# Optimization experiments

Hardware: AMD Instinct MI355X
Metric: run time of the kernel (lower is better)

Reference implementation:

```python
import jax, jax.numpy as jnp
import numpy as np

EPS = 1e-5

def gcn_conv(x, src, dst, W, b, N):
    # PyG GCNConv with self-loops already appended to (src, dst):
    # out = D^{-1/2} (A+I) D^{-1/2} (x @ W) + b
    h = x @ W  # [N, F_out]
    deg = jax.ops.segment_sum(jnp.ones(dst.shape[0], h.dtype), dst, num_segments=N)
    dinv = jnp.where(deg > 0, jax.lax.rsqrt(deg), 0.0)
    norm = dinv[src] * dinv[dst]  # [E']
    msg = h[src] * norm[:, None]  # gather + scale
    out = jax.ops.segment_sum(msg, dst, num_segments=N)  # scatter-add
    return out + b

def layer_norm(x, gamma, beta):
    mu = jnp.mean(x, axis=-1, keepdims=True)
    var = jnp.mean((x - mu) ** 2, axis=-1, keepdims=True)
    return (x - mu) * jax.lax.rsqrt(var + EPS) * gamma + beta

def setup_inputs() -> dict:
    key = jax.random.key(0)
    ks = jax.random.split(key, 12)
    N, E, STEPS = 200000, 12800000, 4
    node = jax.random.normal(ks[0], (N, 3), dtype=jnp.float32)
    edges = jax.random.randint(ks[1], (2, E), 0, N, dtype=jnp.int64)
    W1 = jax.random.normal(ks[2], (3, 6), dtype=jnp.float32) * 0.5
    b1 = jnp.zeros((6,), jnp.float32)
    Wl = jax.random.normal(ks[3], (STEPS, 6, 6), dtype=jnp.float32) * 0.4
    bl = jnp.zeros((STEPS, 6), jnp.float32)
    gamma = jnp.ones((STEPS, 6), jnp.float32)
    beta = jnp.zeros((STEPS, 6), jnp.float32)
    Wfc = jax.random.normal(ks[4], (6, 3), dtype=jnp.float32) * 0.4
    bfc = jnp.zeros((3,), jnp.float32)
    return {"node": node, "edges": edges, "W1": W1, "b1": b1, "Wl": Wl,
            "bl": bl, "gamma": gamma, "beta": beta, "Wfc": Wfc, "bfc": bfc}

def reference(node, edges, W1, b1, Wl, bl, gamma, beta, Wfc, bfc):
    N = node.shape[0]
    loops = jnp.arange(N, dtype=edges.dtype)
    src = jnp.concatenate([edges[0], loops])  # add self-loops once
    dst = jnp.concatenate([edges[1], loops])
    x = gcn_conv(node, src, dst, W1, b1, N)
    steps = Wl.shape[0]
    for i in range(steps):
        x_res = x
        x = gcn_conv(x, src, dst, Wl[i], bl[i], N)
        x = layer_norm(x, gamma[i], beta[i])
        x = x + x_res
        x = jax.nn.relu(x)
    return x @ Wfc + bfc
```

## Files before the change

### kernel.cpp

```cpp
#include <hip/hip_runtime.h>
#include <hip/hip_fp16.h>
#include <cstdint>

#define EPSLN 1e-5f
#define NPB 256
#define NPB_SHIFT 8
#define MAXB 1024
#define TILE 16384
#define SRC_BITS 18
#define SRC_MASK 0x3FFFF
#define FCAP 17664
#define FK 35

__global__ __launch_bounds__(512) void k_init(int* __restrict__ bcur, int B, int cap) {
    int b = blockIdx.x * 512 + threadIdx.x;
    if (b < B) bcur[b] = b * cap;
}

__global__ __launch_bounds__(512) void k_scatter(const int* __restrict__ src,
                                                 const int* __restrict__ dst,
                                                 int* __restrict__ bcur,
                                                 unsigned* __restrict__ packed,
                                                 int E, int B) {
    __shared__ unsigned stg[TILE];
    __shared__ int hist[MAXB];
    __shared__ int lbase[MAXB + 1];
    __shared__ int sm[MAXB];
    int tid = threadIdx.x;
    int i0 = tid, i1 = tid + 512;
    hist[i0] = 0; hist[i1] = 0;
    __syncthreads();

    int beg = blockIdx.x * TILE;
    int end = min(beg + TILE, E);
    int cnt = end - beg;

    unsigned w[32];
    unsigned m[32];

    if (cnt == TILE && ((E & 3) == 0)) {
        const int4* d4 = (const int4*)(dst + beg);
        const int4* s4 = (const int4*)(src + beg);
#pragma unroll
        for (int k = 0; k < 8; ++k) {
            int4 d = d4[tid + k * 512];
            int4 s = s4[tid + k * 512];
            int b0 = d.x >> NPB_SHIFT, b1 = d.y >> NPB_SHIFT;
            int b2 = d.z >> NPB_SHIFT, b3 = d.w >> NPB_SHIFT;
            int r0 = atomicAdd(&hist[b0], 1);
            int r1 = atomicAdd(&hist[b1], 1);
            int r2 = atomicAdd(&hist[b2], 1);
            int r3 = atomicAdd(&hist[b3], 1);
            w[4 * k + 0] = ((unsigned)(d.x & (NPB - 1)) << SRC_BITS) | (unsigned)s.x;
            w[4 * k + 1] = ((unsigned)(d.y & (NPB - 1)) << SRC_BITS) | (unsigned)s.y;
            w[4 * k + 2] = ((unsigned)(d.z & (NPB - 1)) << SRC_BITS) | (unsigned)s.z;
            w[4 * k + 3] = ((unsigned)(d.w & (NPB - 1)) << SRC_BITS) | (unsigned)s.w;
            m[4 * k + 0] = ((unsigned)b0 << 14) | (unsigned)r0;
            m[4 * k + 1] = ((unsigned)b1 << 14) | (unsigned)r1;
            m[4 * k + 2] = ((unsigned)b2 << 14) | (unsigned)r2;
            m[4 * k + 3] = ((unsigned)b3 << 14) | (unsigned)r3;
        }
    } else {
#pragma unroll
        for (int k = 0; k < 32; ++k) {
            int i = beg + tid + k * 512;
            if (i < end) {
                int d = dst[i];
                int s = src[i];
                int bkt = d >> NPB_SHIFT;
                int r = atomicAdd(&hist[bkt], 1);
                w[k] = ((unsigned)(d & (NPB - 1)) << SRC_BITS) | (unsigned)s;
                m[k] = ((unsigned)bkt << 14) | (unsigned)r;
            } else {
                m[k] = 0xFFFFFFFFu;
            }
        }
    }
    __syncthreads();

    int v0 = hist[i0], v1 = hist[i1];
    sm[i0] = v0; sm[i1] = v1;
    __syncthreads();
    for (int off = 1; off < MAXB; off <<= 1) {
        int t0 = (i0 >= off) ? sm[i0 - off] : 0;
        int t1 = (i1 >= off) ? sm[i1 - off] : 0;
        __syncthreads();
        sm[i0] += t0; sm[i1] += t1;
        __syncthreads();
    }
    lbase[i0] = sm[i0] - v0;
    lbase[i1] = sm[i1] - v1;
    if (i0 < B) hist[i0] = v0 ? atomicAdd(&bcur[i0], v0) : 0;
    if (i1 < B) hist[i1] = v1 ? atomicAdd(&bcur[i1], v1) : 0;
    if (tid == 0) lbase[B] = cnt;
    __syncthreads();

#pragma unroll
    for (int k = 0; k < 32; ++k) {
        if (m[k] != 0xFFFFFFFFu) {
            int bkt = (int)(m[k] >> 14);
            int r   = (int)(m[k] & 16383u);
            stg[lbase[bkt] + r] = w[k];
        }
    }
    __syncthreads();

    int grp = tid >> 4;
    int gl  = tid & 15;
    for (int b = grp; b < B; b += 32) {
        int lb = lbase[b];
        int le = lbase[b + 1];
        int gb = hist[b];
        for (int j = lb + gl; j < le; j += 16)
            packed[gb + (j - lb)] = stg[j];
    }
}

__global__ __launch_bounds__(512) void k_fine(const int* __restrict__ bcur,
                                              const unsigned* __restrict__ packed,
                                              int* __restrict__ csr,
                                              int2* __restrict__ ptr2,
                                              float* __restrict__ dinv,
                                              float* __restrict__ sqd,
                                              const float* __restrict__ node,
                                              float* __restrict__ xs3,
                                              int N, int cap) {
    __shared__ unsigned stg[FCAP];
    __shared__ int hist[NPB];
    __shared__ int exs[NPB];
    int b = blockIdx.x;
    int tid = threadIdx.x;
    int beg = b * cap;
    int cnt = min(bcur[b] - beg, FCAP);
    if (tid < NPB) hist[tid] = 0;
    __syncthreads();

    unsigned w[FK];
    int r[FK];
#pragma unroll
    for (int k = 0; k < FK; ++k) {
        int i = tid + k * 512;
        if (i < cnt) {
            w[k] = packed[beg + i];
            r[k] = atomicAdd(&hist[w[k] >> SRC_BITS], 1);
        }
    }
    __syncthreads();

    int hv = 0;
    if (tid < NPB) { hv = hist[tid]; exs[tid] = hv; }
    __syncthreads();
    for (int off = 1; off < NPB; off <<= 1) {
        int t = 0;
        if (tid < NPB && tid >= off) t = exs[tid - off];
        __syncthreads();
        if (tid < NPB) exs[tid] += t;
        __syncthreads();
    }
    if (tid < NPB) {
        int ex = exs[tid] - hv;
        int v = b * NPB + tid;
        if (v < N) {
            ptr2[v] = make_int2(beg + ex, beg + ex + hv);
            float c = (float)(hv + 1);
            float di = rsqrtf(c);
            dinv[v] = di;
            sqd[v] = sqrtf(c);
            xs3[(size_t)v * 4 + 0] = di * node[(size_t)v * 3 + 0];
            xs3[(size_t)v * 4 + 1] = di * node[(size_t)v * 3 + 1];
            xs3[(size_t)v * 4 + 2] = di * node[(size_t)v * 3 + 2];
            xs3[(size_t)v * 4 + 3] = 0.f;
        }
        exs[tid] = ex;
    }
    __syncthreads();

#pragma unroll
    for (int k = 0; k < FK; ++k) {
        int i = tid + k * 512;
        if (i < cnt) {
            int dl = (int)(w[k] >> SRC_BITS);
            stg[exs[dl] + r[k]] = w[k] & SRC_MASK;
        }
    }
    __syncthreads();

    for (int j = tid; j < cnt; j += 512)
        csr[beg + j] = (int)stg[j];
}

template <int MODE>
__global__ __launch_bounds__(512) void k_conv(const int2* __restrict__ ptr2,
                                              const int* __restrict__ csr,
                                              const float* __restrict__ dinv,
                                              const float* __restrict__ sqd,
                                              const float* __restrict__ xs,
                                              const __half* __restrict__ xsh,
                                              const float* __restrict__ W,
                                              const float* __restrict__ b,
                                              const float* __restrict__ gamma,
                                              const float* __restrict__ beta,
                                              const float* __restrict__ Wfc,
                                              const float* __restrict__ bfc,
                                              float* __restrict__ xsout,
                                              __half* __restrict__ xhout,
                                              float* __restrict__ outfc,
                                              int N) {
    constexpr int F = (MODE == 0) ? 3 : 6;
    int wave = threadIdx.x >> 6;
    int lane = threadIdx.x & 63;
    int sub  = lane >> 4;
    int li   = lane & 15;
    int v = (blockIdx.x * 8 + wave) * 4 + sub;
    bool valid = v < N;
    int beg = 0, end = 0;
    if (valid) { int2 p = ptr2[v]; beg = p.x; end = p.y; }

    float a0 = 0.f, a1 = 0.f, a2 = 0.f, a3 = 0.f, a4 = 0.f, a5 = 0.f;
    float xr0 = 0.f, xr1 = 0.f, xr2 = 0.f, xr3 = 0.f, xr4 = 0.f, xr5 = 0.f;
    if constexpr (F == 3) {
        const float4* x4 = (const float4*)xs;
        if (valid && li == 0) { float4 p = x4[v]; a0 += p.x; a1 += p.y; a2 += p.z; }
        int i = beg + li;
        int last = end - 1;
        while (i < end) {
            int i1 = i + 16, i2 = i + 32, i3 = i + 48;
            int j0 = csr[i];
            int j1 = csr[min(i1, last)];
            int j2 = csr[min(i2, last)];
            int j3 = csr[min(i3, last)];
            float4 p0 = x4[j0];
            float4 p1 = x4[j1];
            float4 p2 = x4[j2];
            float4 p3 = x4[j3];
            a0 += p0.x; a1 += p0.y; a2 += p0.z;
            if (i1 < end) { a0 += p1.x; a1 += p1.y; a2 += p1.z; }
            if (i2 < end) { a0 += p2.x; a1 += p2.y; a2 += p2.z; }
            if (i3 < end) { a0 += p3.x; a1 += p3.y; a2 += p3.z; }
            i += 64;
        }
    } else {
        const float4* xh4 = (const float4*)xsh;
        if (valid && li == 0) {
            const float* rp = xs + (size_t)v * 8;
            float4 p = *(const float4*)rp;
            float2 q = *(const float2*)(rp + 4);
            xr0 = p.x; xr1 = p.y; xr2 = p.z; xr3 = p.w; xr4 = q.x; xr5 = q.y;
            a0 += xr0; a1 += xr1; a2 += xr2; a3 += xr3; a4 += xr4; a5 += xr5;
        }
        int i = beg + li;
        int last = end - 1;
        while (i < end) {
            int i1 = i + 16, i2 = i + 32, i3 = i + 48;
            int j0 = csr[i];
            int j1 = csr[min(i1, last)];
            int j2 = csr[min(i2, last)];
            int j3 = csr[min(i3, last)];
            float4 r0 = xh4[j0];
            float4 r1 = xh4[j1];
            float4 r2 = xh4[j2];
            float4 r3 = xh4[j3];
            {
                const __half2* h2 = (const __half2*)&r0;
                float2 p0 = __half22float2(h2[0]);
                float2 p1 = __half22float2(h2[1]);
                float2 p2 = __half22float2(h2[2]);
                a0 += p0.x; a1 += p0.y; a2 += p1.x; a3 += p1.y; a4 += p2.x; a5 += p2.y;
            }
            if (i1 < end) {
                const __half2* h2 = (const __half2*)&r1;
                float2 p0 = __half22float2(h2[0]);
                float2 p1 = __half22float2(h2[1]);
                float2 p2 = __half22float2(h2[2]);
                a0 += p0.x; a1 += p0.y; a2 += p1.x; a3 += p1.y; a4 += p2.x; a5 += p2.y;
            }
            if (i2 < end) {
                const __half2* h2 = (const __half2*)&r2;
                float2 p0 = __half22float2(h2[0]);
                float2 p1 = __half22float2(h2[1]);
                float2 p2 = __half22float2(h2[2]);
                a0 += p0.x; a1 += p0.y; a2 += p1.x; a3 += p1.y; a4 += p2.x; a5 += p2.y;
            }
            if (i3 < end) {
                const __half2* h2 = (const __half2*)&r3;
                float2 p0 = __half22float2(h2[0]);
                float2 p1 = __half22float2(h2[1]);
                float2 p2 = __half22float2(h2[2]);
                a0 += p0.x; a1 += p0.y; a2 += p1.x; a3 += p1.y; a4 += p2.x; a5 += p2.y;
            }
            i += 64;
        }
    }
#pragma unroll
    for (int off = 8; off >= 1; off >>= 1) {
        a0 += __shfl_down(a0, off);
        a1 += __shfl_down(a1, off);
        a2 += __shfl_down(a2, off);
        if constexpr (F == 6) {
            a3 += __shfl_down(a3, off);
            a4 += __shfl_down(a4, off);
            a5 += __shfl_down(a5, off);
        }
    }
    if (li != 0 || !valid) return;

    float di = dinv[v];
    float t[F];
    t[0] = di * a0; t[1] = di * a1; t[2] = di * a2;
    if constexpr (F == 6) { t[3] = di * a3; t[4] = di * a4; t[5] = di * a5; }

    float y[6];
#pragma unroll
    for (int j = 0; j < 6; ++j) {
        float acc = b[j];
#pragma unroll
        for (int k = 0; k < F; ++k) acc += t[k] * W[k * 6 + j];
        y[j] = acc;
    }

    if constexpr (MODE == 0) {
        float* o = xsout + (size_t)v * 8;
        *(float4*)o = make_float4(di * y[0], di * y[1], di * y[2], di * y[3]);
        *(float2*)(o + 4) = make_float2(di * y[4], di * y[5]);
        __half2* oh = (__half2*)(xhout + (size_t)v * 8);
        oh[0] = __floats2half2_rn(di * y[0], di * y[1]);
        oh[1] = __floats2half2_rn(di * y[2], di * y[3]);
        oh[2] = __floats2half2_rn(di * y[4], di * y[5]);
        oh[3] = __floats2half2_rn(0.f, 0.f);
    } else {
        float mu = 0.f;
#pragma unroll
        for (int j = 0; j < 6; ++j) mu += y[j];
        mu *= (1.f / 6.f);
        float var = 0.f;
#pragma unroll
        for (int j = 0; j < 6; ++j) { float dl = y[j] - mu; var += dl * dl; }
        var *= (1.f / 6.f);
        float rs = rsqrtf(var + EPSLN);
        float sq = sqd[v];
        float xr[6] = {xr0, xr1, xr2, xr3, xr4, xr5};
        float r[6];
#pragma unroll
        for (int j = 0; j < 6; ++j) {
            float z = (y[j] - mu) * rs * gamma[j] + beta[j] + xr[j] * sq;
            r[j] = z > 0.f ? z : 0.f;
        }
        if constexpr (MODE == 1) {
            float* o = xsout + (size_t)v * 8;
            *(float4*)o = make_float4(di * r[0], di * r[1], di * r[2], di * r[3]);
            *(float2*)(o + 4) = make_float2(di * r[4], di * r[5]);
            __half2* oh = (__half2*)(xhout + (size_t)v * 8);
            oh[0] = __floats2half2_rn(di * r[0], di * r[1]);
            oh[1] = __floats2half2_rn(di * r[2], di * r[3]);
            oh[2] = __floats2half2_rn(di * r[4], di * r[5]);
            oh[3] = __floats2half2_rn(0.f, 0.f);
        } else {
#pragma unroll
            for (int j = 0; j < 3; ++j) {
                float acc = bfc[j];
#pragma unroll
                for (int k = 0; k < 6; ++k) acc += r[k] * Wfc[k * 3 + j];
                outfc[(size_t)v * 3 + j] = acc;
            }
        }
    }
}

extern "C" void kernel_launch(void* const* d_in, const int* in_sizes, int n_in,
                              void* d_out, int out_size, void* d_ws, size_t ws_size,
                              hipStream_t stream) {
    const float* node  = (const float*)d_in[0];
    const int*   edges = (const int*)d_in[1];
    const float* W1    = (const float*)d_in[2];
    const float* b1    = (const float*)d_in[3];
    const float* Wl    = (const float*)d_in[4];
    const float* bl    = (const float*)d_in[5];
    const float* gamma = (const float*)d_in[6];
    const float* beta  = (const float*)d_in[7];
    const float* Wfc   = (const float*)d_in[8];
    const float* bfc   = (const float*)d_in[9];
    float* out = (float*)d_out;

    const int N     = in_sizes[0] / 3;
    const int E     = in_sizes[1] / 2;
    const int STEPS = in_sizes[4] / 36;
    const int* src = edges;
    const int* dst = edges + E;
    const int B = (N + NPB - 1) / NPB;

    const int mean = E / B;
    int CAP = (mean + 8 * (int)(sqrt((double)mean) + 1) + 255) & ~255;
    if (CAP > FCAP) CAP = FCAP;

    char* ws = (char*)d_ws;
    size_t off = 0;
    auto alloc = [&](size_t bytes) -> void* {
        void* p = ws + off;
        off += (bytes + 255) & ~(size_t)255;
        return p;
    };
    int*      bcur   = (int*)alloc((size_t)B * sizeof(int));
    int2*     ptr2   = (int2*)alloc((size_t)N * sizeof(int2));
    float*    dinv   = (float*)alloc((size_t)N * sizeof(float));
    float*    sqd    = (float*)alloc((size_t)N * sizeof(float));
    unsigned* packed = (unsigned*)alloc((size_t)B * CAP * sizeof(unsigned));
    int*      csr    = (int*)alloc((size_t)B * CAP * sizeof(int));
    float*    xs3    = (float*)alloc((size_t)N * 4 * sizeof(float));
    float*    xsa    = (float*)alloc((size_t)N * 8 * sizeof(float));
    float*    xsb    = (float*)alloc((size_t)N * 8 * sizeof(float));
    __half*   xha    = (__half*)alloc((size_t)N * 8 * sizeof(__half));
    __half*   xhb    = (__half*)alloc((size_t)N * 8 * sizeof(__half));
    (void)ws_size;

    const int gS = (E + TILE - 1) / TILE;
    const int gC = (N + 31) / 32;

    k_init<<<(B + 511) / 512, 512, 0, stream>>>(bcur, B, CAP);
    k_scatter<<<gS, 512, 0, stream>>>(src, dst, bcur, packed, E, B);
    k_fine<<<B, 512, 0, stream>>>(bcur, packed, csr, ptr2, dinv, sqd, node, xs3, N, CAP);

    k_conv<0><<<gC, 512, 0, stream>>>(ptr2, csr, dinv, sqd, xs3, nullptr, W1, b1,
                                      nullptr, nullptr, nullptr, nullptr,
                                      xsa, xha, nullptr, N);

    float* xscur = xsa;   __half* xhcur = xha;
    float* xsnxt = xsb;   __half* xhnxt = xhb;
    for (int i = 0; i < STEPS; ++i) {
        const float* W  = Wl + (size_t)i * 36;
        const float* bb = bl + (size_t)i * 6;
        const float* g  = gamma + (size_t)i * 6;
        const float* be = beta + (size_t)i * 6;
        if (i == STEPS - 1) {
            k_conv<2><<<gC, 512, 0, stream>>>(ptr2, csr, dinv, sqd, xscur, xhcur, W, bb,
                                              g, be, Wfc, bfc, nullptr, nullptr, out, N);
        } else {
            k_conv<1><<<gC, 512, 0, stream>>>(ptr2, csr, dinv, sqd, xscur, xhcur, W, bb,
                                              g, be, nullptr, nullptr, xsnxt, xhnxt, nullptr, N);
        }
        float* t1 = xscur; xscur = xsnxt; xsnxt = t1;
        __half* t2 = xhcur; xhcur = xhnxt; xhnxt = t2;
    }
}
```

Measured before the change: 582.6 us.

## Replace atomic bucket histogram in k_fine with per-thread byte counters and prefix

The fine-grained CSR sort kernel drops shared-memory atomicAdd ranking and instead keeps a private 8-bit counter per (destination, thread) in a 256x260 byte table. Each destination row is prefix-summed across threads to give stable ranks without atomics. Packed edges are read twice with int4 loads instead of being held in registers, and CSR output is written with int4 stores. The block shrinks to 256 threads. Shared memory use grows to about 137 KB, which limits occupancy. The byte counters assume no thread sees more than 255 edges for one destination, which holds given FG*4=72 edges per thread.

```diff
diff --git a/kernel.cpp b/kernel.cpp
--- a/kernel.cpp
+++ b/kernel.cpp
@@ -10,7 +10,8 @@
 #define SRC_BITS 18
 #define SRC_MASK 0x3FFFF
 #define FCAP 17664
-#define FK 35
+#define FG 18
+#define FHS 260
 
 __global__ __launch_bounds__(512) void k_init(int* __restrict__ bcur, int B, int cap) {
     int b = blockIdx.x * 512 + threadIdx.x;
@@ -116,7 +117,7 @@
     }
 }
 
-__global__ __launch_bounds__(512) void k_fine(const int* __restrict__ bcur,
+__global__ __launch_bounds__(256) void k_fine(const int* __restrict__ bcur,
                                               const unsigned* __restrict__ packed,
                                               int* __restrict__ csr,
                                               int2* __restrict__ ptr2,
@@ -125,39 +126,62 @@
                                               const float* __restrict__ node,
                                               float* __restrict__ xs3,
                                               int N, int cap) {
-    __shared__ unsigned stg[FCAP];
-    __shared__ int hist[NPB];
+    __shared__ int stg2[FCAP];
+    __shared__ unsigned char h8[NPB * FHS];
     __shared__ int exs[NPB];
     int b = blockIdx.x;
     int tid = threadIdx.x;
     int beg = b * cap;
     int cnt = min(bcur[b] - beg, FCAP);
-    if (tid < NPB) hist[tid] = 0;
-    __syncthreads();
-
-    unsigned w[FK];
-    int r[FK];
-#pragma unroll
-    for (int k = 0; k < FK; ++k) {
-        int i = tid + k * 512;
-        if (i < cnt) {
-            w[k] = packed[beg + i];
-            r[k] = atomicAdd(&hist[w[k] >> SRC_BITS], 1);
-        }
-    }
-    __syncthreads();
-
-    int hv = 0;
-    if (tid < NPB) { hv = hist[tid]; exs[tid] = hv; }
-    __syncthreads();
+    int ng = (cnt + 3) >> 2;
+
+    unsigned* h32 = (unsigned*)h8;
+    for (int t = tid; t < NPB * FHS / 4; t += 256) h32[t] = 0u;
+    __syncthreads();
+
+    const int4* p4 = (const int4*)(packed + beg);
+#pragma unroll
+    for (int j = 0; j < FG; ++j) {
+        int g = tid + j * 256;
+        if (g < ng) {
+            int4 e = p4[g];
+            int base = 4 * g;
+            unsigned w0 = (unsigned)e.x, w1 = (unsigned)e.y;
+            unsigned w2 = (unsigned)e.z, w3 = (unsigned)e.w;
+            h8[(w0 >> SRC_BITS) * FHS + tid]++;
+            if (base + 1 < cnt) h8[(w1 >> SRC_BITS) * FHS + tid]++;
+            if (base + 2 < cnt) h8[(w2 >> SRC_BITS) * FHS + tid]++;
+            if (base + 3 < cnt) h8[(w3 >> SRC_BITS) * FHS + tid]++;
+        }
+    }
+    __syncthreads();
+
+    int hv;
+    {
+        unsigned* row = (unsigned*)(h8 + tid * FHS);
+        unsigned run = 0;
+#pragma unroll 8
+        for (int wi = 0; wi < 64; ++wi) {
+            unsigned v = row[wi];
+            unsigned n0 = run;
+            unsigned n1 = n0 + (v & 255u);
+            unsigned n2 = n1 + ((v >> 8) & 255u);
+            unsigned n3 = n2 + ((v >> 16) & 255u);
+            run = n3 + (v >> 24);
+            row[wi] = n0 | (n1 << 8) | (n2 << 16) | (n3 << 24);
+        }
+        hv = (int)run;
+        exs[tid] = hv;
+    }
+    __syncthreads();
+
     for (int off = 1; off < NPB; off <<= 1) {
-        int t = 0;
-        if (tid < NPB && tid >= off) t = exs[tid - off];
+        int t = (tid >= off) ? exs[tid - off] : 0;
         __syncthreads();
-        if (tid < NPB) exs[tid] += t;
+        exs[tid] += t;
         __syncthreads();
     }
-    if (tid < NPB) {
+    {
         int ex = exs[tid] - hv;
         int v = b * NPB + tid;
         if (v < N) {
@@ -176,17 +200,35 @@
     __syncthreads();
 
 #pragma unroll
-    for (int k = 0; k < FK; ++k) {
-        int i = tid + k * 512;
-        if (i < cnt) {
-            int dl = (int)(w[k] >> SRC_BITS);
-            stg[exs[dl] + r[k]] = w[k] & SRC_MASK;
-        }
-    }
-    __syncthreads();
-
-    for (int j = tid; j < cnt; j += 512)
-        csr[beg + j] = (int)stg[j];
+    for (int j = 0; j < FG; ++j) {
+        int g = tid + j * 256;
+        if (g < ng) {
+            int4 e = p4[g];
+            int base = 4 * g;
+            unsigned wv[4] = {(unsigned)e.x, (unsigned)e.y, (unsigned)e.z, (unsigned)e.w};
+#pragma unroll
+            for (int k = 0; k < 4; ++k) {
+                if (base + k < cnt) {
+                    unsigned w = wv[k];
+                    int dl = (int)(w >> SRC_BITS);
+                    int hi = dl * FHS + tid;
+                    int r = h8[hi];
+                    h8[hi] = (unsigned char)(r + 1);
+                    stg2[exs[dl] + r] = (int)(w & SRC_MASK);
+                }
+            }
+        }
+    }
+    __syncthreads();
+
+    int4* c4 = (int4*)(csr + beg);
+#pragma unroll
+    for (int j = 0; j < FG; ++j) {
+        int g = tid + j * 256;
+        if (g < ng)
+            c4[g] = make_int4(stg2[4 * g], stg2[4 * g + 1],
+                              stg2[4 * g + 2], stg2[4 * g + 3]);
+    }
 }
 
 template <int MODE>
@@ -417,7 +459,7 @@
 
     k_init<<<(B + 511) / 512, 512, 0, stream>>>(bcur, B, CAP);
     k_scatter<<<gS, 512, 0, stream>>>(src, dst, bcur, packed, E, B);
-    k_fine<<<B, 512, 0, stream>>>(bcur, packed, csr, ptr2, dinv, sqd, node, xs3, N, CAP);
+    k_fine<<<B, 256, 0, stream>>>(bcur, packed, csr, ptr2, dinv, sqd, node, xs3, N, CAP);
 
     k_conv<0><<<gC, 512, 0, stream>>>(ptr2, csr, dinv, sqd, xs3, nullptr, W1, b1,
                                       nullptr, nullptr, nullptr, nullptr,
```

New measurement: 626.6 us. +7.5%, slower.
